# Performance work log

Hardware: AMD Instinct MI355X
Metric: run time of the kernel (lower is better)

Reference implementation:

```python
import jax, jax.numpy as jnp
import numpy as np

N_NODES = 50000
N_EDGES = 1600000
IN_FEATS = 128
HIDDEN = 128
N_CLASSES = 16
N_GRAPHS = 512


def setup_inputs() -> dict:
    key = jax.random.key(0)
    ks = jax.random.split(key, 10)
    features = jax.random.normal(ks[0], (N_NODES, IN_FEATS), dtype=jnp.float32)
    src = jax.random.randint(ks[1], (N_EDGES,), 0, N_NODES, dtype=jnp.int32)
    dst = jax.random.randint(ks[2], (N_EDGES,), 0, N_NODES, dtype=jnp.int32)
    graph_ids = jnp.sort(jax.random.randint(ks[3], (N_NODES,), 0, N_GRAPHS, dtype=jnp.int32))
    # GraphConv weights (glorot-ish scaling) and biases
    W1 = jax.random.normal(ks[4], (IN_FEATS, HIDDEN), dtype=jnp.float32) / np.sqrt(IN_FEATS)
    b1 = jnp.zeros((HIDDEN,), dtype=jnp.float32)
    W2 = jax.random.normal(ks[5], (HIDDEN, HIDDEN), dtype=jnp.float32) / np.sqrt(HIDDEN)
    b2 = jnp.zeros((HIDDEN,), dtype=jnp.float32)
    Wf = jax.random.normal(ks[6], (HIDDEN, N_CLASSES), dtype=jnp.float32) / np.sqrt(HIDDEN)
    bf = jnp.zeros((N_CLASSES,), dtype=jnp.float32)
    return {"features": features, "W1": W1, "b1": b1, "W2": W2, "b2": b2,
            "Wf": Wf, "bf": bf, "src": src, "dst": dst, "graph_ids": graph_ids}


def _graph_conv(h, W, b, src, dst, norm_out, norm_in):
    # DGL GraphConv, norm='both': h' = D_in^{-1/2} * A^T * (D_out^{-1/2} * h) @ W + b
    h = h * norm_out[:, None]              # [N, d] scale by src out-degree
    agg = jax.ops.segment_sum(h[src], dst, num_segments=N_NODES)  # gather-scatter SpMM
    agg = agg * norm_in[:, None]
    return agg @ W + b


def reference(features, W1, b1, W2, b2, Wf, bf, src, dst, graph_ids):
    ones_e = jnp.ones((N_EDGES,), dtype=features.dtype)
    deg_out = jax.ops.segment_sum(ones_e, src, num_segments=N_NODES)
    deg_in = jax.ops.segment_sum(ones_e, dst, num_segments=N_NODES)
    norm_out = jnp.where(deg_out > 0, jax.lax.rsqrt(jnp.maximum(deg_out, 1.0)), 0.0)
    norm_in = jnp.where(deg_in > 0, jax.lax.rsqrt(jnp.maximum(deg_in, 1.0)), 0.0)

    x = jax.nn.relu(_graph_conv(features, W1, b1, src, dst, norm_out, norm_in))
    x = jax.nn.relu(_graph_conv(x, W2, b2, src, dst, norm_out, norm_in))

    # mean_nodes: per-graph mean pooling over batched graph
    sums = jax.ops.segment_sum(x, graph_ids, num_segments=N_GRAPHS)   # [G, d]
    counts = jax.ops.segment_sum(jnp.ones((N_NODES,), dtype=x.dtype), graph_ids,
                                 num_segments=N_GRAPHS)
    pooled = sums / jnp.maximum(counts, 1.0)[:, None]
    return pooled @ Wf + bf
```

## Files before the change

kernel.cpp:

```cpp
#include <hip/hip_runtime.h>

#define N_NODES 50000
#define N_EDGES 1600000
#define FEATS 128
#define N_GRAPHS 512
#define N_CLASSES 16

#define NC 400
#define CE 4000
#define NB 391
#define SLAB 4608
#define CSLAB 5504

typedef __attribute__((ext_vector_type(8))) short bf16x8;
typedef __attribute__((ext_vector_type(4))) float f32x4;

__device__ inline unsigned bf16_rne_bits(float x) {
    unsigned u = __float_as_uint(x);
    return (u + 0x7FFFu + ((u >> 16) & 1u)) >> 16;
}
__device__ inline unsigned pack_bf16(float a, float b) {
    return (bf16_rne_bits(b) << 16) | bf16_rne_bits(a);
}
__device__ inline float bf16lo(unsigned u) { return __uint_as_float(u << 16); }
__device__ inline float bf16hi(unsigned u) { return __uint_as_float(u & 0xFFFF0000u); }

__global__ __launch_bounds__(256) void countrank_kernel(
        const int* __restrict__ src, const int* __restrict__ dst,
        unsigned short* __restrict__ ranksD, unsigned short* __restrict__ ranksS,
        unsigned* __restrict__ cntD, unsigned* __restrict__ cntS) {
    __shared__ unsigned hD[NB], hS[NB];
    for (int i = threadIdx.x; i < NB; i += 256) { hD[i] = 0; hS[i] = 0; }
    __syncthreads();
    int c = blockIdx.x;
    int lo = c * CE;
    for (int i = lo + threadIdx.x; i < lo + CE; i += 256) {
        int d = dst[i];
        int s = src[i];
        ranksD[i] = (unsigned short)atomicAdd(&hD[d >> 7], 1u);
        ranksS[i] = (unsigned short)atomicAdd(&hS[s >> 7], 1u);
    }
    __syncthreads();
    for (int i = threadIdx.x; i < NB; i += 256) {
        cntD[c * NB + i] = hD[i];
        cntS[c * NB + i] = hS[i];
    }
}

__global__ __launch_bounds__(512) void colscan_kernel(
        unsigned* __restrict__ cntD, unsigned* __restrict__ cntS,
        unsigned* __restrict__ totD, unsigned* __restrict__ totS) {
    int bb = blockIdx.x;
    unsigned* cnt = (bb < NB) ? cntD : cntS;
    unsigned* tot = (bb < NB) ? totD : totS;
    int col = (bb < NB) ? bb : bb - NB;
    __shared__ unsigned buf[512];
    int t = threadIdx.x;
    unsigned v = (t < NC) ? cnt[t * NB + col] : 0;
    buf[t] = v;
    __syncthreads();
    for (int off = 1; off < 512; off <<= 1) {
        unsigned add = (t >= off) ? buf[t - off] : 0;
        __syncthreads();
        buf[t] += add;
        __syncthreads();
    }
    if (t < NC) cnt[t * NB + col] = buf[t] - v;
    if (t == NC - 1) tot[col] = buf[t];
}

__global__ __launch_bounds__(256) void scatter_kernel(
        const int* __restrict__ src, const int* __restrict__ dst,
        const unsigned short* __restrict__ ranksD, const unsigned short* __restrict__ ranksS,
        const unsigned* __restrict__ colbaseD, const unsigned* __restrict__ colbaseS,
        unsigned* __restrict__ arenaD, unsigned char* __restrict__ arenaS) {
    __shared__ unsigned cbD[NB], cbS[NB];
    int c = blockIdx.x;
    for (int i = threadIdx.x; i < NB; i += 256) {
        cbD[i] = colbaseD[c * NB + i];
        cbS[i] = colbaseS[c * NB + i];
    }
    __syncthreads();
    int lo = c * CE;
    for (int i = lo + threadIdx.x; i < lo + CE; i += 256) {
        int d = dst[i];
        int s = src[i];
        unsigned posD = (unsigned)(d >> 7) * SLAB + cbD[d >> 7] + ranksD[i];
        arenaD[posD] = (unsigned)s | ((unsigned)(d & 127) << 16);
        unsigned posS = (unsigned)(s >> 7) * SLAB + cbS[s >> 7] + ranksS[i];
        arenaS[posS] = (unsigned char)(s & 127);
    }
}

__global__ __launch_bounds__(256) void finalize_kernel(
        const unsigned* __restrict__ arenaD, const unsigned* __restrict__ totD,
        unsigned short* __restrict__ csr, unsigned* __restrict__ row_start,
        unsigned* __restrict__ cnt_in) {
    int b = blockIdx.x;
    __shared__ unsigned h[128], h2[128], loc[128], sbuf[128];
    __shared__ unsigned short stag[CSLAB];
    int t = threadIdx.x;
    if (t < 128) { h[t] = 0; h2[t] = 0; }
    __syncthreads();
    unsigned nb = totD[b];
    const unsigned* slab = arenaD + (size_t)b * SLAB;
    for (unsigned i = t; i < nb; i += 256) atomicAdd(&h[slab[i] >> 16], 1u);
    __syncthreads();
    unsigned myv = 0;
    if (t < 128) { myv = (h[t] + 7u) & ~7u; sbuf[t] = myv; }
    __syncthreads();
    for (int off = 1; off < 128; off <<= 1) {
        unsigned add = 0;
        if (t < 128 && t >= off) add = sbuf[t - off];
        __syncthreads();
        if (t < 128) sbuf[t] += add;
        __syncthreads();
    }
    if (t < 128) {
        loc[t] = sbuf[t] - myv;
        int dd = b * 128 + t;
        if (dd < N_NODES) {
            cnt_in[dd] = h[t];
            row_start[dd] = (unsigned)b * CSLAB + loc[t];
        }
    }
    __syncthreads();
    for (unsigned i = t; i < nb; i += 256) {
        unsigned e = slab[i];
        unsigned dl = e >> 16;
        unsigned r = atomicAdd(&h2[dl], 1u);
        stag[loc[dl] + r] = (unsigned short)(e & 0xFFFFu);
    }
    __syncthreads();
    unsigned tot_aligned = sbuf[127];
    unsigned short* g = csr + (size_t)b * CSLAB;
    for (unsigned i = t; i < tot_aligned; i += 256) g[i] = stag[i];
}

__global__ __launch_bounds__(256) void degout_kernel(
        const unsigned char* __restrict__ arenaS, const unsigned* __restrict__ totS,
        unsigned* __restrict__ deg_out) {
    int b = blockIdx.x;
    __shared__ unsigned h[128];
    int t = threadIdx.x;
    if (t < 128) h[t] = 0;
    __syncthreads();
    unsigned nb = totS[b];
    const unsigned char* slab = arenaS + (size_t)b * SLAB;
    for (unsigned i = t; i < nb; i += 256) atomicAdd(&h[slab[i]], 1u);
    __syncthreads();
    if (t < 128) {
        int ss = b * 128 + t;
        if (ss < N_NODES) deg_out[ss] = h[t];
    }
}

__global__ __launch_bounds__(256) void wsplit_kernel(
        const float* __restrict__ W1, const float* __restrict__ W2,
        unsigned short* __restrict__ t1h, unsigned short* __restrict__ t1l,
        unsigned short* __restrict__ t2h, unsigned short* __restrict__ t2l) {
    int b = blockIdx.x;
    const float* W = (b < 64) ? W1 : W2;
    unsigned short* th = (b < 64) ? t1h : t2h;
    unsigned short* tl = (b < 64) ? t1l : t2l;
    int idx = (b & 63) * 256 + threadIdx.x;
    int k = idx >> 7;
    int col = idx & 127;
    float w = W[idx];
    unsigned hb = bf16_rne_bits(w);
    float hf = __uint_as_float(hb << 16);
    unsigned lb = bf16_rne_bits(w - hf);
    th[col * 128 + k] = (unsigned short)hb;
    tl[col * 128 + k] = (unsigned short)lb;
}

__global__ void norm_prescale_kernel(const unsigned* __restrict__ deg_out,
                                     const unsigned* __restrict__ cnt_in,
                                     const float* __restrict__ X, unsigned* __restrict__ Xs,
                                     float* __restrict__ norm_in_a, float* __restrict__ norm_out_a,
                                     const int* __restrict__ gids,
                                     int* __restrict__ gstart, int* __restrict__ gend) {
    int gid = blockIdx.x * blockDim.x + threadIdx.x;
    if (gid >= N_NODES * 16) return;
    int node = gid >> 4;
    int c = gid & 15;
    unsigned d0 = deg_out[node];
    float no = d0 > 0 ? rsqrtf((float)d0) : 0.f;
    float4 a0 = *reinterpret_cast<const float4*>(X + (size_t)node * FEATS + c * 8);
    float4 a1 = *reinterpret_cast<const float4*>(X + (size_t)node * FEATS + c * 8 + 4);
    uint4 p;
    p.x = pack_bf16(a0.x * no, a0.y * no);
    p.y = pack_bf16(a0.z * no, a0.w * no);
    p.z = pack_bf16(a1.x * no, a1.y * no);
    p.w = pack_bf16(a1.z * no, a1.w * no);
    *reinterpret_cast<uint4*>(Xs + (size_t)node * (FEATS / 2) + c * 4) = p;
    if (c == 0) {
        norm_out_a[node] = no;
        unsigned d1 = cnt_in[node];
        norm_in_a[node] = d1 > 0 ? rsqrtf((float)d1) : 0.f;
        int g = gids[node];
        if (node == 0 || gids[node - 1] != g) gstart[g] = node;
        if (node == N_NODES - 1 || gids[node + 1] != g) gend[g] = node + 1;
    }
}

__global__ __launch_bounds__(256) void agg_kernel(const unsigned* __restrict__ Xs,
        const unsigned short* __restrict__ csr, const unsigned* __restrict__ row_start,
        const unsigned* __restrict__ cnt_in, unsigned* __restrict__ out) {
    int node = blockIdx.x * 8 + (threadIdx.x >> 5);
    if (node >= N_NODES) return;
    int lane = threadIdx.x & 31;
    unsigned n = cnt_in[node];
    const unsigned short* row = csr + row_start[node];
    const int colu = lane * 2;
    float a0 = 0.f, a1 = 0.f, a2 = 0.f, a3 = 0.f;
    unsigned j = 0;
    for (; j + 8 <= n; j += 8) {
        uint4 iv = *reinterpret_cast<const uint4*>(row + j);
        unsigned s0 = iv.x & 0xFFFFu, s1 = iv.x >> 16;
        unsigned s2 = iv.y & 0xFFFFu, s3 = iv.y >> 16;
        unsigned s4 = iv.z & 0xFFFFu, s5 = iv.z >> 16;
        unsigned s6 = iv.w & 0xFFFFu, s7 = iv.w >> 16;
        uint2 g0 = *reinterpret_cast<const uint2*>(Xs + (size_t)s0 * (FEATS / 2) + colu);
        uint2 g1 = *reinterpret_cast<const uint2*>(Xs + (size_t)s1 * (FEATS / 2) + colu);
        uint2 g2 = *reinterpret_cast<const uint2*>(Xs + (size_t)s2 * (FEATS / 2) + colu);
        uint2 g3 = *reinterpret_cast<const uint2*>(Xs + (size_t)s3 * (FEATS / 2) + colu);
        uint2 g4 = *reinterpret_cast<const uint2*>(Xs + (size_t)s4 * (FEATS / 2) + colu);
        uint2 g5 = *reinterpret_cast<const uint2*>(Xs + (size_t)s5 * (FEATS / 2) + colu);
        uint2 g6 = *reinterpret_cast<const uint2*>(Xs + (size_t)s6 * (FEATS / 2) + colu);
        uint2 g7 = *reinterpret_cast<const uint2*>(Xs + (size_t)s7 * (FEATS / 2) + colu);
        a0 += ((bf16lo(g0.x) + bf16lo(g1.x)) + (bf16lo(g2.x) + bf16lo(g3.x)))
            + ((bf16lo(g4.x) + bf16lo(g5.x)) + (bf16lo(g6.x) + bf16lo(g7.x)));
        a1 += ((bf16hi(g0.x) + bf16hi(g1.x)) + (bf16hi(g2.x) + bf16hi(g3.x)))
            + ((bf16hi(g4.x) + bf16hi(g5.x)) + (bf16hi(g6.x) + bf16hi(g7.x)));
        a2 += ((bf16lo(g0.y) + bf16lo(g1.y)) + (bf16lo(g2.y) + bf16lo(g3.y)))
            + ((bf16lo(g4.y) + bf16lo(g5.y)) + (bf16lo(g6.y) + bf16lo(g7.y)));
        a3 += ((bf16hi(g0.y) + bf16hi(g1.y)) + (bf16hi(g2.y) + bf16hi(g3.y)))
            + ((bf16hi(g4.y) + bf16hi(g5.y)) + (bf16hi(g6.y) + bf16hi(g7.y)));
    }
    for (; j < n; ++j) {
        unsigned s = row[j];
        uint2 g = *reinterpret_cast<const uint2*>(Xs + (size_t)s * (FEATS / 2) + colu);
        a0 += bf16lo(g.x); a1 += bf16hi(g.x); a2 += bf16lo(g.y); a3 += bf16hi(g.y);
    }
    uint2 o;
    o.x = pack_bf16(a0, a1);
    o.y = pack_bf16(a2, a3);
    *reinterpret_cast<uint2*>(out + (size_t)node * (FEATS / 2) + colu) = o;
}

template <bool BF16_OUT>
__global__ __launch_bounds__(256) void gemm_kernel(
        const unsigned* __restrict__ A,
        const unsigned short* __restrict__ Wth, const unsigned short* __restrict__ Wtl,
        const float* __restrict__ bias, const float* __restrict__ norm_in,
        const float* __restrict__ post, float* __restrict__ out_f32,
        unsigned short* __restrict__ out_b16, int n_rows) {
    __shared__ unsigned sWh[128 * 68];
    __shared__ unsigned sWl[128 * 68];
    {
        const uint4* gh = reinterpret_cast<const uint4*>(Wth);
        const uint4* gl = reinterpret_cast<const uint4*>(Wtl);
        for (int i = threadIdx.x; i < 2048; i += 256) {
            int col = i >> 4, q = i & 15;
            *reinterpret_cast<uint4*>(sWh + col * 68 + q * 4) = gh[i];
            *reinterpret_cast<uint4*>(sWl + col * 68 + q * 4) = gl[i];
        }
    }
    __syncthreads();

    const int l = threadIdx.x & 63;
    const int w = threadIdx.x >> 6;
    const int rl = l & 15;
    const int kg = l >> 4;
    const int row0 = blockIdx.x * 64 + w * 16;

    int row_a = row0 + rl;
    if (row_a >= n_rows) row_a = n_rows - 1;
    const uint4* Arow = reinterpret_cast<const uint4*>(A + (size_t)row_a * 64);

    f32x4 acc[8];
#pragma unroll
    for (int ct = 0; ct < 8; ++ct) acc[ct] = (f32x4){0.f, 0.f, 0.f, 0.f};

#pragma unroll
    for (int s = 0; s < 4; ++s) {
        bf16x8 af = __builtin_bit_cast(bf16x8, Arow[4 * s + kg]);
#pragma unroll
        for (int ct = 0; ct < 8; ++ct) {
            int colb = ct * 16 + rl;
            bf16x8 bh = __builtin_bit_cast(bf16x8,
                *reinterpret_cast<const uint4*>(sWh + colb * 68 + 16 * s + 4 * kg));
            bf16x8 bl = __builtin_bit_cast(bf16x8,
                *reinterpret_cast<const uint4*>(sWl + colb * 68 + 16 * s + 4 * kg));
            acc[ct] = __builtin_amdgcn_mfma_f32_16x16x32_bf16(af, bl, acc[ct], 0, 0, 0);
            acc[ct] = __builtin_amdgcn_mfma_f32_16x16x32_bf16(af, bh, acc[ct], 0, 0, 0);
        }
    }

    const int rb = row0 + kg * 4;
    float ni[4], po[4];
#pragma unroll
    for (int j = 0; j < 4; ++j) {
        int r = rb + j;
        bool v = r < n_rows;
        ni[j] = v ? norm_in[r] : 0.f;
        po[j] = (BF16_OUT && v) ? post[r] : 1.f;
    }
#pragma unroll
    for (int ct = 0; ct < 8; ++ct) {
        int col = ct * 16 + rl;
        float bc = bias[col];
#pragma unroll
        for (int j = 0; j < 4; ++j) {
            int r = rb + j;
            if (r < n_rows) {
                float o = fmaxf(fmaf(acc[ct][j], ni[j], bc), 0.f);
                if (BF16_OUT)
                    out_b16[(size_t)r * 128 + col] = (unsigned short)bf16_rne_bits(o * po[j]);
                else
                    out_f32[(size_t)r * 128 + col] = o;
            }
        }
    }
}

__global__ __launch_bounds__(256) void pool_final_kernel(
        const float* __restrict__ H, const int* __restrict__ gstart,
        const int* __restrict__ gend, const float* __restrict__ Wf,
        const float* __restrict__ bf, float* __restrict__ out) {
    int g = blockIdx.x;
    int s = gstart[g];
    int e = gend[g];
    int f = threadIdx.x & 127;
    int h = threadIdx.x >> 7;
    float acc = 0.f;
    for (int r = s + h; r < e; r += 2) acc += H[(size_t)r * FEATS + f];
    __shared__ float tmp[256];
    __shared__ float pooled[FEATS];
    tmp[threadIdx.x] = acc;
    __syncthreads();
    if (threadIdx.x < FEATS) {
        float inv = 1.0f / fmaxf((float)(e - s), 1.0f);
        pooled[threadIdx.x] = (tmp[threadIdx.x] + tmp[threadIdx.x + 128]) * inv;
    }
    __syncthreads();
    if (threadIdx.x < N_CLASSES) {
        int c = threadIdx.x;
        float d = bf[c];
        for (int k = 0; k < FEATS; ++k) d = fmaf(pooled[k], Wf[k * N_CLASSES + c], d);
        out[g * N_CLASSES + c] = d;
    }
}

extern "C" void kernel_launch(void* const* d_in, const int* in_sizes, int n_in,
                              void* d_out, int out_size, void* d_ws, size_t ws_size,
                              hipStream_t stream) {
    const float* features = (const float*)d_in[0];
    const float* W1 = (const float*)d_in[1];
    const float* b1 = (const float*)d_in[2];
    const float* W2 = (const float*)d_in[3];
    const float* b2 = (const float*)d_in[4];
    const float* Wf = (const float*)d_in[5];
    const float* bf = (const float*)d_in[6];
    const int* src = (const int*)d_in[7];
    const int* dst = (const int*)d_in[8];
    const int* gids = (const int*)d_in[9];
    float* out = (float*)d_out;

    char* wp = (char*)d_ws;
    auto alloc = [&wp](size_t bytes) {
        char* p = wp;
        wp += (bytes + 255) & ~(size_t)255;
        return p;
    };
    unsigned* buf0u = (unsigned*)alloc((size_t)N_NODES * 64 * 4);
    float* buf1 = (float*)alloc((size_t)N_NODES * FEATS * 4);
    unsigned* B16 = (unsigned*)buf1;
    unsigned short* B16s = (unsigned short*)buf1;
    float* norm_in_a = (float*)alloc(N_NODES * 4);
    float* norm_out_a = (float*)alloc(N_NODES * 4);
    unsigned* deg_out = (unsigned*)alloc(N_NODES * 4);
    unsigned* cnt_in = (unsigned*)alloc(N_NODES * 4);
    unsigned* row_start = (unsigned*)alloc(N_NODES * 4);
    int* gboth = (int*)alloc(2 * N_GRAPHS * 4);
    int* gstart = gboth;
    int* gend = gboth + N_GRAPHS;
    unsigned short* t1h = (unsigned short*)alloc(4 * 16384 * 2);
    unsigned short* t1l = t1h + 16384;
    unsigned short* t2h = t1l + 16384;
    unsigned short* t2l = t2h + 16384;
    unsigned* cntD = (unsigned*)alloc((size_t)NC * NB * 4);
    unsigned* cntS = (unsigned*)alloc((size_t)NC * NB * 4);
    unsigned* totD = (unsigned*)alloc(NB * 4);
    unsigned* totS = (unsigned*)alloc(NB * 4);
    unsigned* arenaD = (unsigned*)alloc((size_t)NB * SLAB * 4);
    unsigned short* ranksD = (unsigned short*)alloc((size_t)N_EDGES * 2 * 2);
    unsigned short* ranksS = ranksD + N_EDGES;
    unsigned short* csr = ranksD;
    unsigned char* arenaS = (unsigned char*)alloc((size_t)NB * SLAB);

    (void)hipMemsetAsync(gboth, 0, 2 * N_GRAPHS * sizeof(int), stream);

    countrank_kernel<<<NC, 256, 0, stream>>>(src, dst, ranksD, ranksS, cntD, cntS);
    colscan_kernel<<<2 * NB, 512, 0, stream>>>(cntD, cntS, totD, totS);
    scatter_kernel<<<NC, 256, 0, stream>>>(src, dst, ranksD, ranksS, cntD, cntS,
                                           arenaD, arenaS);
    finalize_kernel<<<NB, 256, 0, stream>>>(arenaD, totD, csr, row_start, cnt_in);
    degout_kernel<<<NB, 256, 0, stream>>>(arenaS, totS, deg_out);

    wsplit_kernel<<<128, 256, 0, stream>>>(W1, W2, t1h, t1l, t2h, t2l);
    norm_prescale_kernel<<<(N_NODES * 16 + 255) / 256, 256, 0, stream>>>(
        deg_out, cnt_in, features, B16, norm_in_a, norm_out_a, gids, gstart, gend);

    const int agg_blocks = (N_NODES + 7) / 8;
    const int gemm_blocks = (N_NODES + 63) / 64;

    agg_kernel<<<agg_blocks, 256, 0, stream>>>(B16, csr, row_start, cnt_in, buf0u);
    gemm_kernel<true><<<gemm_blocks, 256, 0, stream>>>(
        buf0u, t1h, t1l, b1, norm_in_a, norm_out_a, nullptr, B16s, N_NODES);

    agg_kernel<<<agg_blocks, 256, 0, stream>>>(B16, csr, row_start, cnt_in, buf0u);
    gemm_kernel<false><<<gemm_blocks, 256, 0, stream>>>(
        buf0u, t2h, t2l, b2, norm_in_a, nullptr, buf1, nullptr, N_NODES);

    pool_final_kernel<<<N_GRAPHS, 256, 0, stream>>>(buf1, gstart, gend, Wf, bf, out);
}
```

Measured before the change: 244.0 us.

## Fuse preprocessing kernels, pack ranks, and split aggregation across feature halves

Folds the weight-split kernel into the count/rank launch and the out-degree histogram into the finalize kernel, cutting two launches. The two 16-bit rank arrays become one packed 32-bit array. The CSR rows are padded with a sentinel zero row (node 50000) so aggregation can drop its scalar tail loop. The aggregation kernel also now runs two blocks per node group, each gathering one 32-bit word per lane for half the features, which doubles the block count and trades wider loads for more parallelism.

```diff
diff --git a/kernel.cpp b/kernel.cpp
--- a/kernel.cpp
+++ b/kernel.cpp
@@ -10,7 +10,8 @@
 #define CE 4000
 #define NB 391
 #define SLAB 4608
-#define CSLAB 5504
+#define CSLAB 5632
+#define ZROW 50000
 
 typedef __attribute__((ext_vector_type(8))) short bf16x8;
 typedef __attribute__((ext_vector_type(4))) float f32x4;
@@ -27,9 +28,27 @@
 
 __global__ __launch_bounds__(256) void countrank_kernel(
         const int* __restrict__ src, const int* __restrict__ dst,
-        unsigned short* __restrict__ ranksD, unsigned short* __restrict__ ranksS,
-        unsigned* __restrict__ cntD, unsigned* __restrict__ cntS) {
+        unsigned* __restrict__ ranks, unsigned* __restrict__ cntD, unsigned* __restrict__ cntS,
+        const float* __restrict__ W1, const float* __restrict__ W2,
+        unsigned short* __restrict__ t1h, unsigned short* __restrict__ t1l,
+        unsigned short* __restrict__ t2h, unsigned short* __restrict__ t2l) {
     __shared__ unsigned hD[NB], hS[NB];
+    if (blockIdx.x >= NC) {
+        int b = blockIdx.x - NC;
+        const float* W = (b < 64) ? W1 : W2;
+        unsigned short* th = (b < 64) ? t1h : t2h;
+        unsigned short* tl = (b < 64) ? t1l : t2l;
+        int idx = (b & 63) * 256 + threadIdx.x;
+        int k = idx >> 7;
+        int col = idx & 127;
+        float w = W[idx];
+        unsigned hb = bf16_rne_bits(w);
+        float hf = __uint_as_float(hb << 16);
+        unsigned lb = bf16_rne_bits(w - hf);
+        th[col * 128 + k] = (unsigned short)hb;
+        tl[col * 128 + k] = (unsigned short)lb;
+        return;
+    }
     for (int i = threadIdx.x; i < NB; i += 256) { hD[i] = 0; hS[i] = 0; }
     __syncthreads();
     int c = blockIdx.x;
@@ -37,8 +56,9 @@
     for (int i = lo + threadIdx.x; i < lo + CE; i += 256) {
         int d = dst[i];
         int s = src[i];
-        ranksD[i] = (unsigned short)atomicAdd(&hD[d >> 7], 1u);
-        ranksS[i] = (unsigned short)atomicAdd(&hS[s >> 7], 1u);
+        unsigned rD = atomicAdd(&hD[d >> 7], 1u);
+        unsigned rS = atomicAdd(&hS[s >> 7], 1u);
+        ranks[i] = rD | (rS << 16);
     }
     __syncthreads();
     for (int i = threadIdx.x; i < NB; i += 256) {
@@ -71,7 +91,7 @@
 
 __global__ __launch_bounds__(256) void scatter_kernel(
         const int* __restrict__ src, const int* __restrict__ dst,
-        const unsigned short* __restrict__ ranksD, const unsigned short* __restrict__ ranksS,
+        const unsigned* __restrict__ ranks,
         const unsigned* __restrict__ colbaseD, const unsigned* __restrict__ colbaseS,
         unsigned* __restrict__ arenaD, unsigned char* __restrict__ arenaS) {
     __shared__ unsigned cbD[NB], cbS[NB];
@@ -85,22 +105,35 @@
     for (int i = lo + threadIdx.x; i < lo + CE; i += 256) {
         int d = dst[i];
         int s = src[i];
-        unsigned posD = (unsigned)(d >> 7) * SLAB + cbD[d >> 7] + ranksD[i];
+        unsigned rr = ranks[i];
+        unsigned posD = (unsigned)(d >> 7) * SLAB + cbD[d >> 7] + (rr & 0xFFFFu);
         arenaD[posD] = (unsigned)s | ((unsigned)(d & 127) << 16);
-        unsigned posS = (unsigned)(s >> 7) * SLAB + cbS[s >> 7] + ranksS[i];
+        unsigned posS = (unsigned)(s >> 7) * SLAB + cbS[s >> 7] + (rr >> 16);
         arenaS[posS] = (unsigned char)(s & 127);
     }
 }
 
 __global__ __launch_bounds__(256) void finalize_kernel(
         const unsigned* __restrict__ arenaD, const unsigned* __restrict__ totD,
+        const unsigned char* __restrict__ arenaS, const unsigned* __restrict__ totS,
         unsigned short* __restrict__ csr, unsigned* __restrict__ row_start,
-        unsigned* __restrict__ cnt_in) {
+        unsigned* __restrict__ cnt_in, unsigned* __restrict__ deg_out) {
     int b = blockIdx.x;
     __shared__ unsigned h[128], h2[128], loc[128], sbuf[128];
     __shared__ unsigned short stag[CSLAB];
     int t = threadIdx.x;
     if (t < 128) { h[t] = 0; h2[t] = 0; }
+    for (int i = t; i < CSLAB; i += 256) stag[i] = (unsigned short)ZROW;
+    __syncthreads();
+    unsigned nbS = totS[b];
+    const unsigned char* slabS = arenaS + (size_t)b * SLAB;
+    for (unsigned i = t; i < nbS; i += 256) atomicAdd(&h2[slabS[i]], 1u);
+    __syncthreads();
+    if (t < 128) {
+        int ss = b * 128 + t;
+        if (ss < N_NODES) deg_out[ss] = h2[t];
+        h2[t] = 0;
+    }
     __syncthreads();
     unsigned nb = totD[b];
     const unsigned* slab = arenaD + (size_t)b * SLAB;
@@ -137,43 +170,6 @@
     for (unsigned i = t; i < tot_aligned; i += 256) g[i] = stag[i];
 }
 
-__global__ __launch_bounds__(256) void degout_kernel(
-        const unsigned char* __restrict__ arenaS, const unsigned* __restrict__ totS,
-        unsigned* __restrict__ deg_out) {
-    int b = blockIdx.x;
-    __shared__ unsigned h[128];
-    int t = threadIdx.x;
-    if (t < 128) h[t] = 0;
-    __syncthreads();
-    unsigned nb = totS[b];
-    const unsigned char* slab = arenaS + (size_t)b * SLAB;
-    for (unsigned i = t; i < nb; i += 256) atomicAdd(&h[slab[i]], 1u);
-    __syncthreads();
-    if (t < 128) {
-        int ss = b * 128 + t;
-        if (ss < N_NODES) deg_out[ss] = h[t];
-    }
-}
-
-__global__ __launch_bounds__(256) void wsplit_kernel(
-        const float* __restrict__ W1, const float* __restrict__ W2,
-        unsigned short* __restrict__ t1h, unsigned short* __restrict__ t1l,
-        unsigned short* __restrict__ t2h, unsigned short* __restrict__ t2l) {
-    int b = blockIdx.x;
-    const float* W = (b < 64) ? W1 : W2;
-    unsigned short* th = (b < 64) ? t1h : t2h;
-    unsigned short* tl = (b < 64) ? t1l : t2l;
-    int idx = (b & 63) * 256 + threadIdx.x;
-    int k = idx >> 7;
-    int col = idx & 127;
-    float w = W[idx];
-    unsigned hb = bf16_rne_bits(w);
-    float hf = __uint_as_float(hb << 16);
-    unsigned lb = bf16_rne_bits(w - hf);
-    th[col * 128 + k] = (unsigned short)hb;
-    tl[col * 128 + k] = (unsigned short)lb;
-}
-
 __global__ void norm_prescale_kernel(const unsigned* __restrict__ deg_out,
                                      const unsigned* __restrict__ cnt_in,
                                      const float* __restrict__ X, unsigned* __restrict__ Xs,
@@ -181,9 +177,14 @@
                                      const int* __restrict__ gids,
                                      int* __restrict__ gstart, int* __restrict__ gend) {
     int gid = blockIdx.x * blockDim.x + threadIdx.x;
-    if (gid >= N_NODES * 16) return;
+    if (gid >= (N_NODES + 1) * 16) return;
     int node = gid >> 4;
     int c = gid & 15;
+    if (node >= N_NODES) {
+        uint4 z = {0u, 0u, 0u, 0u};
+        *reinterpret_cast<uint4*>(Xs + (size_t)node * (FEATS / 2) + c * 4) = z;
+        return;
+    }
     unsigned d0 = deg_out[node];
     float no = d0 > 0 ? rsqrtf((float)d0) : 0.f;
     float4 a0 = *reinterpret_cast<const float4*>(X + (size_t)node * FEATS + c * 8);
@@ -207,46 +208,36 @@
 __global__ __launch_bounds__(256) void agg_kernel(const unsigned* __restrict__ Xs,
         const unsigned short* __restrict__ csr, const unsigned* __restrict__ row_start,
         const unsigned* __restrict__ cnt_in, unsigned* __restrict__ out) {
-    int node = blockIdx.x * 8 + (threadIdx.x >> 5);
+    int b = blockIdx.x;
+    int h = b & 1;
+    int node = (b >> 1) * 8 + (threadIdx.x >> 5);
     if (node >= N_NODES) return;
     int lane = threadIdx.x & 31;
     unsigned n = cnt_in[node];
     const unsigned short* row = csr + row_start[node];
-    const int colu = lane * 2;
-    float a0 = 0.f, a1 = 0.f, a2 = 0.f, a3 = 0.f;
-    unsigned j = 0;
-    for (; j + 8 <= n; j += 8) {
+    const unsigned base = h * 32 + lane;
+    float alo = 0.f, ahi = 0.f;
+    unsigned n8 = (n + 7u) & ~7u;
+    for (unsigned j = 0; j < n8; j += 8) {
         uint4 iv = *reinterpret_cast<const uint4*>(row + j);
         unsigned s0 = iv.x & 0xFFFFu, s1 = iv.x >> 16;
         unsigned s2 = iv.y & 0xFFFFu, s3 = iv.y >> 16;
         unsigned s4 = iv.z & 0xFFFFu, s5 = iv.z >> 16;
         unsigned s6 = iv.w & 0xFFFFu, s7 = iv.w >> 16;
-        uint2 g0 = *reinterpret_cast<const uint2*>(Xs + (size_t)s0 * (FEATS / 2) + colu);
-        uint2 g1 = *reinterpret_cast<const uint2*>(Xs + (size_t)s1 * (FEATS / 2) + colu);
-        uint2 g2 = *reinterpret_cast<const uint2*>(Xs + (size_t)s2 * (FEATS / 2) + colu);
-        uint2 g3 = *reinterpret_cast<const uint2*>(Xs + (size_t)s3 * (FEATS / 2) + colu);
-        uint2 g4 = *reinterpret_cast<const uint2*>(Xs + (size_t)s4 * (FEATS / 2) + colu);
-        uint2 g5 = *reinterpret_cast<const uint2*>(Xs + (size_t)s5 * (FEATS / 2) + colu);
-        uint2 g6 = *reinterpret_cast<const uint2*>(Xs + (size_t)s6 * (FEATS / 2) + colu);
-        uint2 g7 = *reinterpret_cast<const uint2*>(Xs + (size_t)s7 * (FEATS / 2) + colu);
-        a0 += ((bf16lo(g0.x) + bf16lo(g1.x)) + (bf16lo(g2.x) + bf16lo(g3.x)))
-            + ((bf16lo(g4.x) + bf16lo(g5.x)) + (bf16lo(g6.x) + bf16lo(g7.x)));
-        a1 += ((bf16hi(g0.x) + bf16hi(g1.x)) + (bf16hi(g2.x) + bf16hi(g3.x)))
-            + ((bf16hi(g4.x) + bf16hi(g5.x)) + (bf16hi(g6.x) + bf16hi(g7.x)));
-        a2 += ((bf16lo(g0.y) + bf16lo(g1.y)) + (bf16lo(g2.y) + bf16lo(g3.y)))
-            + ((bf16lo(g4.y) + bf16lo(g5.y)) + (bf16lo(g6.y) + bf16lo(g7.y)));
-        a3 += ((bf16hi(g0.y) + bf16hi(g1.y)) + (bf16hi(g2.y) + bf16hi(g3.y)))
-            + ((bf16hi(g4.y) + bf16hi(g5.y)) + (bf16hi(g6.y) + bf16hi(g7.y)));
-    }
-    for (; j < n; ++j) {
-        unsigned s = row[j];
-        uint2 g = *reinterpret_cast<const uint2*>(Xs + (size_t)s * (FEATS / 2) + colu);
-        a0 += bf16lo(g.x); a1 += bf16hi(g.x); a2 += bf16lo(g.y); a3 += bf16hi(g.y);
-    }
-    uint2 o;
-    o.x = pack_bf16(a0, a1);
-    o.y = pack_bf16(a2, a3);
-    *reinterpret_cast<uint2*>(out + (size_t)node * (FEATS / 2) + colu) = o;
+        unsigned g0 = Xs[(size_t)s0 * 64 + base];
+        unsigned g1 = Xs[(size_t)s1 * 64 + base];
+        unsigned g2 = Xs[(size_t)s2 * 64 + base];
+        unsigned g3 = Xs[(size_t)s3 * 64 + base];
+        unsigned g4 = Xs[(size_t)s4 * 64 + base];
+        unsigned g5 = Xs[(size_t)s5 * 64 + base];
+        unsigned g6 = Xs[(size_t)s6 * 64 + base];
+        unsigned g7 = Xs[(size_t)s7 * 64 + base];
+        alo += ((bf16lo(g0) + bf16lo(g1)) + (bf16lo(g2) + bf16lo(g3)))
+             + ((bf16lo(g4) + bf16lo(g5)) + (bf16lo(g6) + bf16lo(g7)));
+        ahi += ((bf16hi(g0) + bf16hi(g1)) + (bf16hi(g2) + bf16hi(g3)))
+             + ((bf16hi(g4) + bf16hi(g5)) + (bf16hi(g6) + bf16hi(g7)));
+    }
+    out[(size_t)node * 64 + base] = pack_bf16(alo, ahi);
 }
 
 template <bool BF16_OUT>
@@ -374,8 +365,8 @@
         wp += (bytes + 255) & ~(size_t)255;
         return p;
     };
-    unsigned* buf0u = (unsigned*)alloc((size_t)N_NODES * 64 * 4);
-    float* buf1 = (float*)alloc((size_t)N_NODES * FEATS * 4);
+    unsigned* buf0u = (unsigned*)alloc(((size_t)N_NODES + 1) * 64 * 4);
+    float* buf1 = (float*)alloc((size_t)N_NODES * FEATS * 4 + 256);
     unsigned* B16 = (unsigned*)buf1;
     unsigned short* B16s = (unsigned short*)buf1;
     float* norm_in_a = (float*)alloc(N_NODES * 4);
@@ -395,25 +386,23 @@
     unsigned* totD = (unsigned*)alloc(NB * 4);
     unsigned* totS = (unsigned*)alloc(NB * 4);
     unsigned* arenaD = (unsigned*)alloc((size_t)NB * SLAB * 4);
-    unsigned short* ranksD = (unsigned short*)alloc((size_t)N_EDGES * 2 * 2);
-    unsigned short* ranksS = ranksD + N_EDGES;
-    unsigned short* csr = ranksD;
+    unsigned* ranks = (unsigned*)alloc((size_t)N_EDGES * 4);
+    unsigned short* csr = (unsigned short*)ranks;
     unsigned char* arenaS = (unsigned char*)alloc((size_t)NB * SLAB);
 
     (void)hipMemsetAsync(gboth, 0, 2 * N_GRAPHS * sizeof(int), stream);
 
-    countrank_kernel<<<NC, 256, 0, stream>>>(src, dst, ranksD, ranksS, cntD, cntS);
+    countrank_kernel<<<NC + 128, 256, 0, stream>>>(src, dst, ranks, cntD, cntS,
+                                                   W1, W2, t1h, t1l, t2h, t2l);
     colscan_kernel<<<2 * NB, 512, 0, stream>>>(cntD, cntS, totD, totS);
-    scatter_kernel<<<NC, 256, 0, stream>>>(src, dst, ranksD, ranksS, cntD, cntS,
-                                           arenaD, arenaS);
-    finalize_kernel<<<NB, 256, 0, stream>>>(arenaD, totD, csr, row_start, cnt_in);
-    degout_kernel<<<NB, 256, 0, stream>>>(arenaS, totS, deg_out);
-
-    wsplit_kernel<<<128, 256, 0, stream>>>(W1, W2, t1h, t1l, t2h, t2l);
-    norm_prescale_kernel<<<(N_NODES * 16 + 255) / 256, 256, 0, stream>>>(
+    scatter_kernel<<<NC, 256, 0, stream>>>(src, dst, ranks, cntD, cntS, arenaD, arenaS);
+    finalize_kernel<<<NB, 256, 0, stream>>>(arenaD, totD, arenaS, totS,
+                                            csr, row_start, cnt_in, deg_out);
+
+    norm_prescale_kernel<<<((N_NODES + 1) * 16 + 255) / 256, 256, 0, stream>>>(
         deg_out, cnt_in, features, B16, norm_in_a, norm_out_a, gids, gstart, gend);
 
-    const int agg_blocks = (N_NODES + 7) / 8;
+    const int agg_blocks = 2 * ((N_NODES + 7) / 8);
     const int gemm_blocks = (N_NODES + 63) / 64;
 
     agg_kernel<<<agg_blocks, 256, 0, stream>>>(B16, csr, row_start, cnt_in, buf0u);
```

Result: faster. 219.5 us (-10.0%).
